# Optimization experiments

Hardware: AMD Instinct MI355X
Metric: run time of the kernel (lower is better)

## Reference

```python
import jax, jax.numpy as jnp
import numpy as np

# ---- problem constants (from init_kwargs) ----
B, NJ = 65536, 32
TARGET_LINKS = (8, 16, 24, 32)
POS_W, ORI_W, POSE_W = 1.0, 0.5, 1.0
LIMIT_W, REST_W = 10.0, 0.1
BASE_POS_W, BASE_ORI_W = 5.0, 5.0

# ---- SE3 math (pose = [t(3), quat xyzw(4)]) ----

def quat_mul(q1, q2):
    v1, w1 = q1[..., :3], q1[..., 3:4]
    v2, w2 = q2[..., :3], q2[..., 3:4]
    w = w1 * w2 - jnp.sum(v1 * v2, -1, keepdims=True)
    v = w1 * v2 + w2 * v1 + jnp.cross(v1, v2)
    return jnp.concatenate([v, w], -1)

def quat_rotate(q, t):
    v, w = q[..., :3], q[..., 3:4]
    return t + 2.0 * jnp.cross(v, jnp.cross(v, t) + w * t)

def se3_compose(T1, T2):
    t1, q1 = T1[..., :3], T1[..., 3:]
    t2, q2 = T2[..., :3], T2[..., 3:]
    return jnp.concatenate([t1 + quat_rotate(q1, t2), quat_mul(q1, q2)], -1)

def se3_inverse(T):
    t, q = T[..., :3], T[..., 3:]
    qinv = jnp.concatenate([-q[..., :3], q[..., 3:4]], -1)
    return jnp.concatenate([-quat_rotate(qinv, t), qinv], -1)

def quat_log(q):
    # canonicalize to w >= 0 (shortest rotation)
    q = jnp.where(q[..., 3:4] < 0.0, -q, q)
    v, w = q[..., :3], q[..., 3:4]
    nv2 = jnp.sum(v * v, -1, keepdims=True)
    nv = jnp.sqrt(jnp.maximum(nv2, 1e-14))
    angle = 2.0 * jnp.arctan2(nv, w)
    small = nv < 1e-6
    w_safe = jnp.where(jnp.abs(w) > 1e-8, w, 1.0)
    scale = jnp.where(small, 2.0 / w_safe, angle / nv)
    return v * scale  # phi, |phi| = rotation angle

def se3_log(T):
    # returns 6-vector [rho(3), phi(3)]
    t, q = T[..., :3], T[..., 3:]
    phi = quat_log(q)
    th2 = jnp.sum(phi * phi, -1, keepdims=True)
    th = jnp.sqrt(jnp.maximum(th2, 1e-14))
    small = th < 1e-4
    ths = jnp.where(small, 1.0, th)  # safe theta for non-small branch
    a = jnp.where(small,
                  1.0 / 12.0 + th2 / 720.0,
                  (1.0 - ths * jnp.sin(ths) / (2.0 * (1.0 - jnp.cos(ths)))) / (ths * ths))
    # rho = V^{-1}(phi) @ t, with hat(phi) x = cross(phi, x)
    pt = jnp.cross(phi, t)
    rho = t - 0.5 * pt + a * jnp.cross(phi, pt)
    return jnp.concatenate([rho, phi], -1)

def forward_kinematics(cfg, base, joint_offsets, joint_axes):
    # cfg [B, NJ], base [B,7] -> fk [B, NJ+1, 7]
    def step(T, inp):
        off, ax, th = inp  # [7], [3], [B]
        T = se3_compose(T, off[None, :])
        half = 0.5 * th[:, None]
        jq = jnp.concatenate([ax[None, :] * jnp.sin(half), jnp.cos(half)], -1)  # [B,4]
        # compose with pure-rotation joint transform (zero translation)
        T = jnp.concatenate([T[..., :3], quat_mul(T[..., 3:], jq)], -1)
        return T, T
    _, poses = jax.lax.scan(step, base, (joint_offsets, joint_axes, cfg.T))  # [NJ,B,7]
    return jnp.concatenate([base[:, None, :], jnp.swapaxes(poses, 0, 1)], 1)

# ---- inputs ----

def _rand_pose(key, shape):
    k1, k2 = jax.random.split(key)
    t = jax.random.normal(k1, shape + (3,), dtype=jnp.float32) * 0.5
    q = jax.random.normal(k2, shape + (4,), dtype=jnp.float32)
    q = q / jnp.linalg.norm(q, axis=-1, keepdims=True)
    return jnp.concatenate([t, q], -1)

def setup_inputs() -> dict:
    key = jax.random.key(0)
    ks = jax.random.split(key, 9)
    cfg = jax.random.normal(ks[0], (B, NJ), dtype=jnp.float32) * 0.3
    default_base = _rand_pose(ks[1], ())
    base = _rand_pose(ks[2], (B,))
    target_poses = _rand_pose(ks[3], (len(TARGET_LINKS),))
    joint_offsets = _rand_pose(ks[4], (NJ,))
    ax = jax.random.normal(ks[5], (NJ, 3), dtype=jnp.float32)
    joint_axes = ax / jnp.linalg.norm(ax, axis=-1, keepdims=True)
    rest_cfg = jax.random.normal(ks[6], (NJ,), dtype=jnp.float32) * 0.2
    joint_lower = -jnp.abs(jax.random.normal(ks[7], (NJ,), dtype=jnp.float32)) - 1.0
    joint_upper = jnp.abs(jax.random.normal(ks[8], (NJ,), dtype=jnp.float32)) + 1.0
    return dict(cfg=cfg, base=base, target_poses=target_poses, default_base=default_base,
                rest_cfg=rest_cfg, joint_offsets=joint_offsets, joint_axes=joint_axes,
                joint_lower=joint_lower, joint_upper=joint_upper)

# ---- forward ----

def reference(cfg, base, target_poses, default_base, rest_cfg,
              joint_offsets, joint_axes, joint_lower, joint_upper):
    fk = forward_kinematics(cfg, base, joint_offsets, joint_axes)  # [B, NJ+1, 7]
    actual = fk[:, jnp.array(TARGET_LINKS), :]                     # [B, T, 7]
    T_err = se3_compose(se3_inverse(target_poses)[None, :, :], actual)
    log_err = se3_log(T_err)                                       # [B, T, 6]
    w6 = jnp.concatenate([jnp.full((3,), POS_W, jnp.float32),
                          jnp.full((3,), ORI_W, jnp.float32)]) * POSE_W
    pose_res = (log_err * w6).reshape(cfg.shape[0], -1)            # [B, 6T]
    limit_res = (jnp.maximum(cfg - joint_upper, 0.0) + jnp.minimum(cfg - joint_lower, 0.0)) * LIMIT_W
    rest_res = (cfg - rest_cfg) * REST_W
    base_err = se3_log(se3_compose(se3_inverse(default_base)[None, :], base))  # [B,6]
    base_res = jnp.concatenate([base_err[:, :3] * BASE_POS_W, base_err[:, 3:] * BASE_ORI_W], -1)
    return jnp.concatenate([pose_res, limit_res, rest_res, base_res], -1)  # [B, 6T+2NJ+6]
```

## Files before the change

### kernel.cpp

```cpp
#include <hip/hip_runtime.h>

#define NJ 32
#define ROWS_PER_BLK 64
#define BLK 256
#define NB 65536

struct V3 { float x, y, z; };
struct Q4 { float x, y, z, w; };

__device__ __forceinline__ V3 v3cross(V3 a, V3 b) {
    V3 r;
    r.x = a.y * b.z - a.z * b.y;
    r.y = a.z * b.x - a.x * b.z;
    r.z = a.x * b.y - a.y * b.x;
    return r;
}

__device__ __forceinline__ Q4 qmul(Q4 a, Q4 b) {
    Q4 r;
    r.x = a.w * b.x + b.w * a.x + (a.y * b.z - a.z * b.y);
    r.y = a.w * b.y + b.w * a.y + (a.z * b.x - a.x * b.z);
    r.z = a.w * b.z + b.w * a.z + (a.x * b.y - a.y * b.x);
    r.w = a.w * b.w - (a.x * b.x + a.y * b.y + a.z * b.z);
    return r;
}

__device__ __forceinline__ V3 qrot(Q4 q, V3 t) {
    V3 v = {q.x, q.y, q.z};
    V3 u = v3cross(v, t);
    u.x += q.w * t.x; u.y += q.w * t.y; u.z += q.w * t.z;
    V3 c = v3cross(v, u);
    V3 r = {t.x + 2.f * c.x, t.y + 2.f * c.y, t.z + 2.f * c.z};
    return r;
}

__device__ __forceinline__ V3 quat_log(Q4 q) {
    float s = (q.w < 0.f) ? -1.f : 1.f;
    float x = q.x * s, y = q.y * s, z = q.z * s, w = q.w * s;
    float nv2 = x * x + y * y + z * z;
    float nv = sqrtf(fmaxf(nv2, 1e-14f));
    float angle = 2.f * atan2f(nv, w);
    float w_safe = (fabsf(w) > 1e-8f) ? w : 1.f;
    float scale = (nv < 1e-6f) ? (2.f / w_safe) : (angle / nv);
    V3 r = {x * scale, y * scale, z * scale};
    return r;
}

__device__ __forceinline__ void se3_log(V3 t, Q4 q, float* o6) {
    V3 phi = quat_log(q);
    float th2 = phi.x * phi.x + phi.y * phi.y + phi.z * phi.z;
    float th = sqrtf(fmaxf(th2, 1e-14f));
    bool small = th < 1e-4f;
    float ths = small ? 1.f : th;
    float sn = __sinf(ths), cs = __cosf(ths);
    float a_big = (1.f - ths * sn / (2.f * (1.f - cs))) / (ths * ths);
    float a = small ? (1.f / 12.f + th2 / 720.f) : a_big;
    V3 pt = v3cross(phi, t);
    V3 ppt = v3cross(phi, pt);
    o6[0] = t.x - 0.5f * pt.x + a * ppt.x;
    o6[1] = t.y - 0.5f * pt.y + a * ppt.y;
    o6[2] = t.z - 0.5f * pt.z + a * ppt.z;
    o6[3] = phi.x;
    o6[4] = phi.y;
    o6[5] = phi.z;
}

__global__ __launch_bounds__(BLK) void ik_kernel(
    const float* __restrict__ cfg,
    const float* __restrict__ base,
    const float* __restrict__ tposes,
    const float* __restrict__ dbase,
    const float* __restrict__ restc,
    const float* __restrict__ joff,
    const float* __restrict__ jaxes,
    const float* __restrict__ jlo,
    const float* __restrict__ jup,
    float* __restrict__ out)
{
    __shared__ float s_mt[NJ][3];
    __shared__ float s_oq[NJ][4];
    __shared__ float s_ax[NJ][3];
    __shared__ float s_lo[NJ];
    __shared__ float s_up[NJ];
    __shared__ float s_rest[NJ];
    __shared__ float s_ti[4][7];
    __shared__ float s_dbi[7];
    __shared__ __align__(8)  float s_base[ROWS_PER_BLK * 7];
    __shared__ __align__(16) float s_out[ROWS_PER_BLK * 94];

    const int tid = threadIdx.x;

    if (tid < NJ) {
        const int j = tid;
        s_mt[j][0] = joff[j * 7 + 0];
        s_mt[j][1] = joff[j * 7 + 1];
        s_mt[j][2] = joff[j * 7 + 2];
        s_oq[j][0] = joff[j * 7 + 3];
        s_oq[j][1] = joff[j * 7 + 4];
        s_oq[j][2] = joff[j * 7 + 5];
        s_oq[j][3] = joff[j * 7 + 6];
        s_ax[j][0] = jaxes[j * 3 + 0];
        s_ax[j][1] = jaxes[j * 3 + 1];
        s_ax[j][2] = jaxes[j * 3 + 2];
        s_lo[j] = jlo[j];
        s_up[j] = jup[j];
        s_rest[j] = restc[j];
    } else if (tid < 36) {
        const int i = tid - 32;
        V3 t = {tposes[i * 7 + 0], tposes[i * 7 + 1], tposes[i * 7 + 2]};
        Q4 q = {tposes[i * 7 + 3], tposes[i * 7 + 4], tposes[i * 7 + 5], tposes[i * 7 + 6]};
        Q4 qi = {-q.x, -q.y, -q.z, q.w};
        V3 rt = qrot(qi, t);
        s_ti[i][0] = -rt.x; s_ti[i][1] = -rt.y; s_ti[i][2] = -rt.z;
        s_ti[i][3] = qi.x;  s_ti[i][4] = qi.y;  s_ti[i][5] = qi.z;  s_ti[i][6] = qi.w;
    } else if (tid == 36) {
        V3 t = {dbase[0], dbase[1], dbase[2]};
        Q4 q = {dbase[3], dbase[4], dbase[5], dbase[6]};
        Q4 qi = {-q.x, -q.y, -q.z, q.w};
        V3 rt = qrot(qi, t);
        s_dbi[0] = -rt.x; s_dbi[1] = -rt.y; s_dbi[2] = -rt.z;
        s_dbi[3] = qi.x;  s_dbi[4] = qi.y;  s_dbi[5] = qi.z;  s_dbi[6] = qi.w;
    }
    if (tid < 224) {
        reinterpret_cast<float2*>(s_base)[tid] =
            reinterpret_cast<const float2*>(base + (size_t)blockIdx.x * ROWS_PER_BLK * 7)[tid];
    }
    __syncthreads();

    const int r   = tid >> 2;
    const int sub = tid & 3;
    const size_t b = (size_t)blockIdx.x * ROWS_PER_BLK + r;
    const int j0 = sub * 8;

    float cf[8];
    {
        const float4* cp = reinterpret_cast<const float4*>(cfg + b * NJ + j0);
        float4 c0 = cp[0], c1 = cp[1];
        cf[0] = c0.x; cf[1] = c0.y; cf[2] = c0.z; cf[3] = c0.w;
        cf[4] = c1.x; cf[5] = c1.y; cf[6] = c1.z; cf[7] = c1.w;
    }

    V3 St; Q4 Sq;
    {
        float half = 0.5f * cf[0];
        float sh = __sinf(half), ch = __cosf(half);
        Q4 jq = {s_ax[j0][0] * sh, s_ax[j0][1] * sh, s_ax[j0][2] * sh, ch};
        Q4 oq = {s_oq[j0][0], s_oq[j0][1], s_oq[j0][2], s_oq[j0][3]};
        Sq = qmul(oq, jq);
        St.x = s_mt[j0][0]; St.y = s_mt[j0][1]; St.z = s_mt[j0][2];
    }
    #pragma unroll
    for (int k = 1; k < 8; ++k) {
        const int j = j0 + k;
        float half = 0.5f * cf[k];
        float sh = __sinf(half), ch = __cosf(half);
        Q4 jq = {s_ax[j][0] * sh, s_ax[j][1] * sh, s_ax[j][2] * sh, ch};
        Q4 oq = {s_oq[j][0], s_oq[j][1], s_oq[j][2], s_oq[j][3]};
        Q4 mq = qmul(oq, jq);
        V3 mt = {s_mt[j][0], s_mt[j][1], s_mt[j][2]};
        V3 rt = qrot(Sq, mt);
        St.x += rt.x; St.y += rt.y; St.z += rt.z;
        Sq = qmul(Sq, mq);
    }

    #pragma unroll
    for (int d = 1; d <= 2; d <<= 1) {
        V3 Ut; Q4 Uq;
        Ut.x = __shfl_up(St.x, d, 4);
        Ut.y = __shfl_up(St.y, d, 4);
        Ut.z = __shfl_up(St.z, d, 4);
        Uq.x = __shfl_up(Sq.x, d, 4);
        Uq.y = __shfl_up(Sq.y, d, 4);
        Uq.z = __shfl_up(Sq.z, d, 4);
        Uq.w = __shfl_up(Sq.w, d, 4);
        V3 ct = qrot(Uq, St);
        ct.x += Ut.x; ct.y += Ut.y; ct.z += Ut.z;
        Q4 cq = qmul(Uq, Sq);
        bool take = (sub >= d);
        St.x = take ? ct.x : St.x; St.y = take ? ct.y : St.y; St.z = take ? ct.z : St.z;
        Sq.x = take ? cq.x : Sq.x; Sq.y = take ? cq.y : Sq.y;
        Sq.z = take ? cq.z : Sq.z; Sq.w = take ? cq.w : Sq.w;
    }

    V3 b_t = {s_base[r * 7 + 0], s_base[r * 7 + 1], s_base[r * 7 + 2]};
    Q4 b_q = {s_base[r * 7 + 3], s_base[r * 7 + 4], s_base[r * 7 + 5], s_base[r * 7 + 6]};
    V3 Tt = qrot(b_q, St);
    Tt.x += b_t.x; Tt.y += b_t.y; Tt.z += b_t.z;
    Q4 Tq = qmul(b_q, Sq);

    float* o = s_out + r * 94;

    {
        V3 it = {s_ti[sub][0], s_ti[sub][1], s_ti[sub][2]};
        Q4 iq = {s_ti[sub][3], s_ti[sub][4], s_ti[sub][5], s_ti[sub][6]};
        V3 et = qrot(iq, Tt);
        et.x += it.x; et.y += it.y; et.z += it.z;
        Q4 eq = qmul(iq, Tq);
        float l6[6];
        se3_log(et, eq, l6);
        o[sub * 6 + 0] = l6[0];
        o[sub * 6 + 1] = l6[1];
        o[sub * 6 + 2] = l6[2];
        o[sub * 6 + 3] = l6[3] * 0.5f;
        o[sub * 6 + 4] = l6[4] * 0.5f;
        o[sub * 6 + 5] = l6[5] * 0.5f;
    }

    #pragma unroll
    for (int k = 0; k < 8; ++k) {
        const int j = j0 + k;
        float c = cf[k];
        float lim = (fmaxf(c - s_up[j], 0.f) + fminf(c - s_lo[j], 0.f)) * 10.f;
        o[24 + j] = lim;
        o[56 + j] = (c - s_rest[j]) * 0.1f;
    }

    if (sub == 0) {
        V3 it = {s_dbi[0], s_dbi[1], s_dbi[2]};
        Q4 iq = {s_dbi[3], s_dbi[4], s_dbi[5], s_dbi[6]};
        V3 et = qrot(iq, b_t);
        et.x += it.x; et.y += it.y; et.z += it.z;
        Q4 eq = qmul(iq, b_q);
        float l6[6];
        se3_log(et, eq, l6);
        o[88] = l6[0] * 5.f;
        o[89] = l6[1] * 5.f;
        o[90] = l6[2] * 5.f;
        o[91] = l6[3] * 5.f;
        o[92] = l6[4] * 5.f;
        o[93] = l6[5] * 5.f;
    }

    __syncthreads();

    {
        const uint4* src = reinterpret_cast<const uint4*>(s_out);
        uint4* dst = reinterpret_cast<uint4*>(out + (size_t)blockIdx.x * ROWS_PER_BLK * 94);
        #pragma unroll
        for (int i = 0; i < 6; ++i) {
            int idx = i * BLK + tid;
            if (idx < 1504) dst[idx] = src[idx];
        }
    }
}

extern "C" void kernel_launch(void* const* d_in, const int* in_sizes, int n_in,
                              void* d_out, int out_size, void* d_ws, size_t ws_size,
                              hipStream_t stream) {
    const float* cfg   = (const float*)d_in[0];
    const float* base  = (const float*)d_in[1];
    const float* tp    = (const float*)d_in[2];
    const float* db    = (const float*)d_in[3];
    const float* rest  = (const float*)d_in[4];
    const float* joff  = (const float*)d_in[5];
    const float* jax   = (const float*)d_in[6];
    const float* jlo   = (const float*)d_in[7];
    const float* jup   = (const float*)d_in[8];
    float* out = (float*)d_out;

    ik_kernel<<<NB / ROWS_PER_BLK, BLK, 0, stream>>>(cfg, base, tp, db, rest, joff, jax, jlo, jup, out);
}
```

Baseline: 91.93 us.

## Halve block size, pack joint constants for vector LDS loads, polynomial atan2

Rows per block drop from 64 to 32 and threads per block from 256 to 128, doubling the grid. Joint offsets and axes are packed into one padded 12-float record per joint, permuted so each sub-lane reads with three float4 LDS loads. atan2f in quat_log is replaced by a minimax polynomial valid for non-negative arguments, which relies on w being canonicalized to be non-negative and introduces small approximation error. The aim is to cut LDS traffic and transcendental cost and to improve occupancy and tail balance.

```diff
diff --git a/kernel.cpp b/kernel.cpp
--- a/kernel.cpp
+++ b/kernel.cpp
@@ -1,8 +1,8 @@
 #include <hip/hip_runtime.h>
 
 #define NJ 32
-#define ROWS_PER_BLK 64
-#define BLK 256
+#define RPB 32
+#define BLK 128
 #define NB 65536
 
 struct V3 { float x, y, z; };
@@ -34,12 +34,26 @@
     return r;
 }
 
+__device__ __forceinline__ float atan2_pos(float y, float x) {
+    float mn = fminf(y, x), mx = fmaxf(y, x);
+    float t = mn / mx;
+    float t2 = t * t;
+    float p = -0.01172120f;
+    p = p * t2 + 0.05265332f;
+    p = p * t2 - 0.11643287f;
+    p = p * t2 + 0.19354346f;
+    p = p * t2 - 0.33262347f;
+    p = p * t2 + 0.99997726f;
+    float r = p * t;
+    return (y > x) ? (1.57079632679f - r) : r;
+}
+
 __device__ __forceinline__ V3 quat_log(Q4 q) {
     float s = (q.w < 0.f) ? -1.f : 1.f;
     float x = q.x * s, y = q.y * s, z = q.z * s, w = q.w * s;
     float nv2 = x * x + y * y + z * z;
     float nv = sqrtf(fmaxf(nv2, 1e-14f));
-    float angle = 2.f * atan2f(nv, w);
+    float angle = 2.f * atan2_pos(nv, w);
     float w_safe = (fabsf(w) > 1e-8f) ? w : 1.f;
     float scale = (nv < 1e-6f) ? (2.f / w_safe) : (angle / nv);
     V3 r = {x * scale, y * scale, z * scale};
@@ -77,31 +91,32 @@
     const float* __restrict__ jup,
     float* __restrict__ out)
 {
-    __shared__ float s_mt[NJ][3];
-    __shared__ float s_oq[NJ][4];
-    __shared__ float s_ax[NJ][3];
+    __shared__ __align__(16) float s_jc[NJ][12];
     __shared__ float s_lo[NJ];
     __shared__ float s_up[NJ];
     __shared__ float s_rest[NJ];
     __shared__ float s_ti[4][7];
     __shared__ float s_dbi[7];
-    __shared__ __align__(8)  float s_base[ROWS_PER_BLK * 7];
-    __shared__ __align__(16) float s_out[ROWS_PER_BLK * 94];
+    __shared__ __align__(8)  float s_base[RPB * 7];
+    __shared__ __align__(16) float s_out[RPB * 94];
 
     const int tid = threadIdx.x;
 
     if (tid < NJ) {
         const int j = tid;
-        s_mt[j][0] = joff[j * 7 + 0];
-        s_mt[j][1] = joff[j * 7 + 1];
-        s_mt[j][2] = joff[j * 7 + 2];
-        s_oq[j][0] = joff[j * 7 + 3];
-        s_oq[j][1] = joff[j * 7 + 4];
-        s_oq[j][2] = joff[j * 7 + 5];
-        s_oq[j][3] = joff[j * 7 + 6];
-        s_ax[j][0] = jaxes[j * 3 + 0];
-        s_ax[j][1] = jaxes[j * 3 + 1];
-        s_ax[j][2] = jaxes[j * 3 + 2];
+        const int rj = ((j & 7) << 2) | (j >> 3);
+        s_jc[rj][0] = joff[j * 7 + 0];
+        s_jc[rj][1] = joff[j * 7 + 1];
+        s_jc[rj][2] = joff[j * 7 + 2];
+        s_jc[rj][3] = joff[j * 7 + 3];
+        s_jc[rj][4] = joff[j * 7 + 4];
+        s_jc[rj][5] = joff[j * 7 + 5];
+        s_jc[rj][6] = joff[j * 7 + 6];
+        s_jc[rj][7] = jaxes[j * 3 + 0];
+        s_jc[rj][8] = jaxes[j * 3 + 1];
+        s_jc[rj][9] = jaxes[j * 3 + 2];
+        s_jc[rj][10] = 0.f;
+        s_jc[rj][11] = 0.f;
         s_lo[j] = jlo[j];
         s_up[j] = jup[j];
         s_rest[j] = restc[j];
@@ -121,15 +136,15 @@
         s_dbi[0] = -rt.x; s_dbi[1] = -rt.y; s_dbi[2] = -rt.z;
         s_dbi[3] = qi.x;  s_dbi[4] = qi.y;  s_dbi[5] = qi.z;  s_dbi[6] = qi.w;
     }
-    if (tid < 224) {
+    if (tid < 112) {
         reinterpret_cast<float2*>(s_base)[tid] =
-            reinterpret_cast<const float2*>(base + (size_t)blockIdx.x * ROWS_PER_BLK * 7)[tid];
+            reinterpret_cast<const float2*>(base + (size_t)blockIdx.x * RPB * 7)[tid];
     }
     __syncthreads();
 
     const int r   = tid >> 2;
     const int sub = tid & 3;
-    const size_t b = (size_t)blockIdx.x * ROWS_PER_BLK + r;
+    const size_t b = (size_t)blockIdx.x * RPB + r;
     const int j0 = sub * 8;
 
     float cf[8];
@@ -141,26 +156,25 @@
     }
 
     V3 St; Q4 Sq;
-    {
-        float half = 0.5f * cf[0];
-        float sh = __sinf(half), ch = __cosf(half);
-        Q4 jq = {s_ax[j0][0] * sh, s_ax[j0][1] * sh, s_ax[j0][2] * sh, ch};
-        Q4 oq = {s_oq[j0][0], s_oq[j0][1], s_oq[j0][2], s_oq[j0][3]};
-        Sq = qmul(oq, jq);
-        St.x = s_mt[j0][0]; St.y = s_mt[j0][1]; St.z = s_mt[j0][2];
-    }
     #pragma unroll
-    for (int k = 1; k < 8; ++k) {
-        const int j = j0 + k;
+    for (int k = 0; k < 8; ++k) {
+        const int rj = (k << 2) | sub;
+        const float4* jp = reinterpret_cast<const float4*>(s_jc[rj]);
+        float4 f0 = jp[0], f1 = jp[1], f2 = jp[2];
+        V3 mt = {f0.x, f0.y, f0.z};
+        Q4 oq = {f0.w, f1.x, f1.y, f1.z};
+        float ax = f1.w, ay = f2.x, az = f2.y;
         float half = 0.5f * cf[k];
         float sh = __sinf(half), ch = __cosf(half);
-        Q4 jq = {s_ax[j][0] * sh, s_ax[j][1] * sh, s_ax[j][2] * sh, ch};
-        Q4 oq = {s_oq[j][0], s_oq[j][1], s_oq[j][2], s_oq[j][3]};
+        Q4 jq = {ax * sh, ay * sh, az * sh, ch};
         Q4 mq = qmul(oq, jq);
-        V3 mt = {s_mt[j][0], s_mt[j][1], s_mt[j][2]};
-        V3 rt = qrot(Sq, mt);
-        St.x += rt.x; St.y += rt.y; St.z += rt.z;
-        Sq = qmul(Sq, mq);
+        if (k == 0) {
+            St = mt; Sq = mq;
+        } else {
+            V3 rt = qrot(Sq, mt);
+            St.x += rt.x; St.y += rt.y; St.z += rt.z;
+            Sq = qmul(Sq, mq);
+        }
     }
 
     #pragma unroll
@@ -235,11 +249,11 @@
 
     {
         const uint4* src = reinterpret_cast<const uint4*>(s_out);
-        uint4* dst = reinterpret_cast<uint4*>(out + (size_t)blockIdx.x * ROWS_PER_BLK * 94);
+        uint4* dst = reinterpret_cast<uint4*>(out + (size_t)blockIdx.x * RPB * 94);
         #pragma unroll
         for (int i = 0; i < 6; ++i) {
             int idx = i * BLK + tid;
-            if (idx < 1504) dst[idx] = src[idx];
+            if (idx < 752) dst[idx] = src[idx];
         }
     }
 }
@@ -258,5 +272,5 @@
     const float* jup   = (const float*)d_in[8];
     float* out = (float*)d_out;
 
-    ik_kernel<<<NB / ROWS_PER_BLK, BLK, 0, stream>>>(cfg, base, tp, db, rest, joff, jax, jlo, jup, out);
-}
+    ik_kernel<<<NB / RPB, BLK, 0, stream>>>(cfg, base, tp, db, rest, joff, jax, jlo, jup, out);
+}
```

Result: slower. 96.41 us (+4.9%).
